# Kernel tuning notes

Measured on AMD Instinct MI355X. Metric: run time of the kernel, lower is better.

Reference implementation:

```python
import jax, jax.numpy as jnp
import numpy as np

D = 512            # model size
H = 8              # num_heads
HD = D // H        # head_size = 64
WIN = 7            # num_keys (payload tokens per window)
QNB = 5            # query_nb for 'mean' aggregation
SCALE = D ** -0.5  # NOTE: torch module scales by size**-0.5, not head_size**-0.5
EPS = 1e-5


def setup_inputs() -> dict:
    key = jax.random.key(0)
    ks = jax.random.split(key, 12)
    B, M = 8, 4096
    w = lambda i: jax.random.normal(ks[i], (D, D), jnp.float32) * 0.02
    return {
        "k": jax.random.normal(ks[0], (B, M, D), jnp.float32),
        "v": jax.random.normal(ks[1], (B, M, D), jnp.float32),
        "q": jax.random.normal(ks[2], (B, M, D), jnp.float32),
        "query_len": 3584,
        "Wk": w(3), "bk": jnp.zeros((D,), jnp.float32),
        "Wv": w(4), "bv": jnp.zeros((D,), jnp.float32),
        "Wq": w(5), "bq": jnp.zeros((D,), jnp.float32),
        "ln_g": jnp.ones((D,), jnp.float32), "ln_b": jnp.zeros((D,), jnp.float32),
        "Wpq": w(6), "bpq": jnp.zeros((D,), jnp.float32),
        "Wpk": w(7), "bpk": jnp.zeros((D,), jnp.float32),
        "Wo": w(8), "bo": jnp.zeros((D,), jnp.float32),
    }


def reference(k, v, q, query_len, Wk, bk, Wv, bv, Wq, bq, ln_g, ln_b, Wpq, bpq, Wpk, bpk, Wo, bo):
    B, M, _ = k.shape
    win_num = -(-query_len // WIN)     # ceil
    per_win = M // win_num

    k = k @ Wk + bk
    v = v @ Wv + bv
    q = q @ Wq + bq

    # 'mean' query aggregation: AvgPool1d(kernel=QNB, stride=1, pad=QNB//2),
    # count_include_pad=True => always divide by QNB (zero-padded)
    qp = jnp.pad(q, ((0, 0), (QNB // 2, QNB // 2), (0, 0)))
    q = sum(qp[:, j:j + M] for j in range(QNB)) / QNB

    # ---- stage 1: DSA (local attention inside each window of per_win tokens)
    resh = lambda x: x.reshape(B, win_num, per_win, H, HD).transpose(0, 1, 3, 2, 4)
    dq, dk, dv = resh(q), resh(k), resh(v)                       # [B,W,H,p,hd]
    attn = jax.nn.softmax(jnp.einsum('bwhqd,bwhkd->bwhqk', dq, dk) * SCALE, axis=-1)
    out = jnp.einsum('bwhqk,bwhkd->bwhqd', attn, dv)
    out = out.transpose(0, 1, 3, 2, 4).reshape(B, win_num, per_win, D)

    win_tok = out[:, :, 0, :]          # [B, W, D] window summary tokens
    attn_x = out[:, :, 1:, :]

    # LayerNorm + exact GELU on window tokens
    mu = win_tok.mean(-1, keepdims=True)
    var = ((win_tok - mu) ** 2).mean(-1, keepdims=True)
    win_tok = (win_tok - mu) / jnp.sqrt(var + EPS) * ln_g + ln_b
    win_tok = jax.nn.gelu(win_tok, approximate=False)

    # ---- stage 2: PSA (attention over window summary tokens)
    pq = (win_tok @ Wpq + bpq).reshape(B, win_num, H, HD).transpose(0, 2, 1, 3)  # [B,H,W,hd]
    pk = (win_tok @ Wpk + bpk).reshape(B, win_num, H, HD).transpose(0, 2, 1, 3)
    pv = attn_x.reshape(B, win_num, WIN, H, HD).transpose(0, 3, 1, 2, 4)
    pv = pv.reshape(B, H, win_num, WIN * HD)

    pattn = jax.nn.softmax(jnp.einsum('bhqd,bhkd->bhqk', pq, pk) * SCALE, axis=-1)
    pout = jnp.einsum('bhqk,bhkd->bhqd', pattn, pv)
    pout = pout.transpose(0, 2, 1, 3).reshape(B, win_num, H, WIN, HD)
    pout = pout.transpose(0, 1, 3, 2, 4).reshape(B, win_num, WIN, D)

    out = (pout + attn_x).reshape(B, win_num * WIN, D)[:, :query_len, :]
    return out @ Wo + bo
```

## Files before the change

kernel.cpp:

```cpp
#include <hip/hip_runtime.h>
#include <hip/hip_bf16.h>
#include <math.h>

#define SCALE_ 0.04419417382415922f
#define EPS_  1e-5f

typedef unsigned short u16;
typedef __attribute__((ext_vector_type(8))) short     bf16x8;
typedef __attribute__((ext_vector_type(4))) float     f32x4;
typedef __attribute__((ext_vector_type(8))) unsigned short u16x8;
typedef __attribute__((ext_vector_type(4))) unsigned short u16x4;

__device__ __forceinline__ u16 f2b(float f) {
  union { float f; unsigned int u; } x; x.f = f;
  unsigned int u = x.u;
  return (u16)((u + 0x7FFFu + ((u >> 16) & 1u)) >> 16);
}
__device__ __forceinline__ float b2f(u16 h) {
  union { unsigned int u; float f; } x; x.u = ((unsigned int)h) << 16;
  return x.f;
}
__device__ __forceinline__ void gload_lds16(const void* g, void* l) {
  __builtin_amdgcn_global_load_lds(
      (const __attribute__((address_space(1))) void*)g,
      (__attribute__((address_space(3))) void*)l, 16, 0, 0);
}

__global__ __launch_bounds__(256) void wconv(
    const float* W0, const float* W1, const float* W2,
    const float* W3, const float* W4, const float* W5, u16* wt)
{
  const float* W;
  switch (blockIdx.z) {
    case 0: W = W0; break; case 1: W = W1; break; case 2: W = W2; break;
    case 3: W = W3; break; case 4: W = W4; break; default: W = W5; break;
  }
  u16* Wt = wt + (size_t)blockIdx.z * 262144;
  const int k0 = blockIdx.x * 64, n0 = blockIdx.y * 64;
  __shared__ float T[64][68];
  const int tid = threadIdx.x;
#pragma unroll
  for (int it = 0; it < 4; ++it) {
    int L = it * 256 + tid;
    int r = L >> 4, cg = L & 15;
    float4 v = *reinterpret_cast<const float4*>(W + (size_t)(k0 + r) * 512 + n0 + cg * 4);
    T[r][cg * 4 + 0] = v.x; T[r][cg * 4 + 1] = v.y;
    T[r][cg * 4 + 2] = v.z; T[r][cg * 4 + 3] = v.w;
  }
  __syncthreads();
#pragma unroll
  for (int it = 0; it < 2; ++it) {
    int L = it * 256 + tid;
    int rn = L >> 3, kg = L & 7;
    u16x8 o;
#pragma unroll
    for (int e = 0; e < 8; ++e) o[e] = f2b(T[kg * 8 + e][rn]);
    *(u16x8*)(Wt + (size_t)(n0 + rn) * 512 + k0 + kg * 8) = o;
  }
}

__global__ __launch_bounds__(512) void gemm_proj(
    const float* A0, const u16* Bt0, const float* bi0, u16* C0,
    const float* A1, const u16* Bt1, const float* bi1, u16* C1,
    const float* A2, const u16* Bt2, const float* bi2, u16* C2)
{
  const float *A, *bias; const u16* Bt; u16* C;
  if (blockIdx.z == 0)      { A = A0; Bt = Bt0; bias = bi0; C = C0; }
  else if (blockIdx.z == 1) { A = A1; Bt = Bt1; bias = bi1; C = C1; }
  else                      { A = A2; Bt = Bt2; bias = bi2; C = C2; }

  __shared__ u16 As[8192];
  __shared__ u16 Bs[32768];
  const int tid = threadIdx.x;
  const int lane = tid & 63, wid = tid >> 6;
  const int wr = wid >> 2, wcn = wid & 3;
  const int l15 = lane & 15, lh = lane >> 4, l7 = lane & 7;
  const int m0 = blockIdx.x * 128;

  const f32x4 fz = {0.f, 0.f, 0.f, 0.f};
  f32x4 acc[4][8];
#pragma unroll
  for (int m = 0; m < 4; ++m)
#pragma unroll
    for (int n = 0; n < 8; ++n) acc[m][n] = fz;

  int aoff[2], boff[2];
#pragma unroll
  for (int kh = 0; kh < 2; ++kh) {
    int slot = ((kh * 4 + lh) ^ l7) << 4;
    aoff[kh] = (wr * 64 + l15) * 128 + slot;
    boff[kh] = (wcn * 128 + l15) * 128 + slot;
  }

  for (int k0 = 0; k0 < 512; k0 += 64) {
    __syncthreads();
#pragma unroll
    for (int it = 0; it < 8; ++it) {
      int L = it * 512 + tid;
      int r = L >> 3, s = L & 7;
      int c = s ^ (r & 7);
      gload_lds16(Bt + (size_t)r * 512 + k0 + c * 8,
                  (char*)Bs + (it * 512 + wid * 64) * 16);
    }
    float4 xa[2], xb[2];
#pragma unroll
    for (int it = 0; it < 2; ++it) {
      int L = it * 512 + tid;
      int r = L >> 3, s = L & 7;
      int c = s ^ (r & 7);
      const float* ga = A + (size_t)(m0 + r) * 512 + k0 + c * 8;
      xa[it] = *reinterpret_cast<const float4*>(ga);
      xb[it] = *reinterpret_cast<const float4*>(ga + 4);
    }
#pragma unroll
    for (int it = 0; it < 2; ++it) {
      int L = it * 512 + tid;
      u16x8 o;
      o[0] = f2b(xa[it].x); o[1] = f2b(xa[it].y);
      o[2] = f2b(xa[it].z); o[3] = f2b(xa[it].w);
      o[4] = f2b(xb[it].x); o[5] = f2b(xb[it].y);
      o[6] = f2b(xb[it].z); o[7] = f2b(xb[it].w);
      *(u16x8*)((char*)As + L * 16) = o;
    }
    __syncthreads();
#pragma unroll
    for (int kh = 0; kh < 2; ++kh) {
      bf16x8 af[4], bfr[8];
#pragma unroll
      for (int m = 0; m < 4; ++m)
        af[m] = *(const bf16x8*)((const char*)As + aoff[kh] + m * 2048);
#pragma unroll
      for (int n = 0; n < 8; ++n)
        bfr[n] = *(const bf16x8*)((const char*)Bs + boff[kh] + n * 2048);
#pragma unroll
      for (int m = 0; m < 4; ++m)
#pragma unroll
        for (int n = 0; n < 8; ++n)
          acc[m][n] = __builtin_amdgcn_mfma_f32_16x16x32_bf16(af[m], bfr[n], acc[m][n], 0, 0, 0);
    }
  }

  const int gn0 = wcn * 128 + l15;
  float bv[8];
#pragma unroll
  for (int n = 0; n < 8; ++n) bv[n] = bias[gn0 + n * 16];
#pragma unroll
  for (int m = 0; m < 4; ++m)
#pragma unroll
    for (int reg = 0; reg < 4; ++reg) {
      int gm = m0 + wr * 64 + m * 16 + lh * 4 + reg;
#pragma unroll
      for (int n = 0; n < 8; ++n)
        C[(size_t)gm * 512 + gn0 + n * 16] = f2b(acc[m][n][reg] + bv[n]);
    }
}

__global__ __launch_bounds__(512) void gemm_out(
    const u16* __restrict__ A, const u16* __restrict__ Bt,
    const float* __restrict__ bias, float* __restrict__ C)
{
  __shared__ u16 As[2][4096];
  __shared__ u16 Bs[2][16384];
  const int tid = threadIdx.x;
  const int lane = tid & 63, wid = tid >> 6;
  const int wr = wid >> 2, wcn = wid & 3;
  const int l15 = lane & 15, lh = lane >> 4;
  const int sx = (l15 >> 1) & 3;
  const int m0 = blockIdx.x * 128;
  const int rr = tid >> 2, sp = tid & 3;
  const int ssw = sp ^ ((rr >> 1) & 3);

  const f32x4 fz = {0.f, 0.f, 0.f, 0.f};
  f32x4 acc[4][8];
#pragma unroll
  for (int m = 0; m < 4; ++m)
#pragma unroll
    for (int n = 0; n < 8; ++n) acc[m][n] = fz;

  const int aoff0 = (wr * 64 + l15) * 64 + ((lh ^ sx) << 4);
  const int boff0 = (wcn * 128 + l15) * 64 + ((lh ^ sx) << 4);

  {
#pragma unroll
    for (int it = 0; it < 4; ++it)
      gload_lds16(Bt + (size_t)(it * 128 + rr) * 512 + ssw * 8,
                  (char*)Bs[0] + (it * 512 + wid * 64) * 16);
    gload_lds16(A + (size_t)(m0 + rr) * 512 + ssw * 8,
                (char*)As[0] + (wid * 64) * 16);
  }
  __syncthreads();

#pragma unroll 2
  for (int t = 0; t < 16; ++t) {
    const int cur = t & 1, nxt = cur ^ 1;
    if (t < 15) {
      const int k0 = (t + 1) * 32;
#pragma unroll
      for (int it = 0; it < 4; ++it)
        gload_lds16(Bt + (size_t)(it * 128 + rr) * 512 + k0 + ssw * 8,
                    (char*)Bs[nxt] + (it * 512 + wid * 64) * 16);
      gload_lds16(A + (size_t)(m0 + rr) * 512 + k0 + ssw * 8,
                  (char*)As[nxt] + (wid * 64) * 16);
    }
    bf16x8 af[4], bfr[8];
#pragma unroll
    for (int m = 0; m < 4; ++m)
      af[m] = *(const bf16x8*)((const char*)As[cur] + aoff0 + m * 1024);
#pragma unroll
    for (int n = 0; n < 8; ++n)
      bfr[n] = *(const bf16x8*)((const char*)Bs[cur] + boff0 + n * 1024);
#pragma unroll
    for (int m = 0; m < 4; ++m)
#pragma unroll
      for (int n = 0; n < 8; ++n)
        acc[m][n] = __builtin_amdgcn_mfma_f32_16x16x32_bf16(af[m], bfr[n], acc[m][n], 0, 0, 0);
    __syncthreads();
  }

  const int gn0 = wcn * 128 + l15;
  float bv[8];
#pragma unroll
  for (int n = 0; n < 8; ++n) bv[n] = bias[gn0 + n * 16];
#pragma unroll
  for (int m = 0; m < 4; ++m)
#pragma unroll
    for (int reg = 0; reg < 4; ++reg) {
      int gm = m0 + wr * 64 + m * 16 + lh * 4 + reg;
#pragma unroll
      for (int n = 0; n < 8; ++n)
        C[(size_t)gm * 512 + gn0 + n * 16] = acc[m][n][reg] + bv[n];
    }
}

__global__ __launch_bounds__(256) void gemm_pp(
    const u16* __restrict__ A,
    const u16* __restrict__ Bt0, const float* __restrict__ bi0, u16* __restrict__ C0,
    const u16* __restrict__ Bt1, const float* __restrict__ bi1, u16* __restrict__ C1)
{
  const u16* Bt; const float* bias; u16* C;
  if (blockIdx.z == 0) { Bt = Bt0; bias = bi0; C = C0; }
  else                 { Bt = Bt1; bias = bi1; C = C1; }

  __shared__ u16 As[8192];
  __shared__ u16 Bs[8192];
  const int tid = threadIdx.x;
  const int lane = tid & 63, wid = tid >> 6;
  const int wr = wid >> 1, wc = wid & 1;
  const int l15 = lane & 15, lh = lane >> 4, l7 = lane & 7;
  const int m0 = blockIdx.x * 128, n0 = blockIdx.y * 128;

  const f32x4 fz = {0.f, 0.f, 0.f, 0.f};
  f32x4 acc[4][4];
#pragma unroll
  for (int m = 0; m < 4; ++m)
#pragma unroll
    for (int n = 0; n < 4; ++n) acc[m][n] = fz;

  int aoff[2], boff[2];
#pragma unroll
  for (int kh = 0; kh < 2; ++kh) {
    int slot = ((kh * 4 + lh) ^ l7) << 4;
    aoff[kh] = (wr * 64 + l15) * 128 + slot;
    boff[kh] = (wc * 64 + l15) * 128 + slot;
  }

  for (int k0 = 0; k0 < 512; k0 += 64) {
    __syncthreads();
#pragma unroll
    for (int it = 0; it < 4; ++it) {
      int L = it * 256 + tid;
      int r = L >> 3, s = L & 7;
      int c = s ^ (r & 7);
      gload_lds16(A  + (size_t)(m0 + r) * 512 + k0 + c * 8,
                  (char*)As + (it * 256 + wid * 64) * 16);
      gload_lds16(Bt + (size_t)(n0 + r) * 512 + k0 + c * 8,
                  (char*)Bs + (it * 256 + wid * 64) * 16);
    }
    __syncthreads();
#pragma unroll
    for (int kh = 0; kh < 2; ++kh) {
      bf16x8 af[4], bfr[4];
#pragma unroll
      for (int m = 0; m < 4; ++m)
        af[m] = *(const bf16x8*)((const char*)As + aoff[kh] + m * 2048);
#pragma unroll
      for (int n = 0; n < 4; ++n)
        bfr[n] = *(const bf16x8*)((const char*)Bs + boff[kh] + n * 2048);
#pragma unroll
      for (int m = 0; m < 4; ++m)
#pragma unroll
        for (int n = 0; n < 4; ++n)
          acc[m][n] = __builtin_amdgcn_mfma_f32_16x16x32_bf16(af[m], bfr[n], acc[m][n], 0, 0, 0);
    }
  }

  const int gn0 = n0 + wc * 64 + l15;
  float bv[4];
#pragma unroll
  for (int n = 0; n < 4; ++n) bv[n] = bias[gn0 + n * 16];
#pragma unroll
  for (int m = 0; m < 4; ++m)
#pragma unroll
    for (int reg = 0; reg < 4; ++reg) {
      int gm = m0 + wr * 64 + m * 16 + lh * 4 + reg;
#pragma unroll
      for (int n = 0; n < 4; ++n)
        C[(size_t)gm * 512 + gn0 + n * 16] = f2b(acc[m][n][reg] + bv[n]);
    }
}

__global__ __launch_bounds__(256) void qk_mfma(
    const u16* __restrict__ pq, const u16* __restrict__ pk, u16* __restrict__ expS)
{
  __shared__ u16 As[8192];
  __shared__ u16 Bs[8192];
  const int tid = threadIdx.x;
  const int lane = tid & 63, wid = tid >> 6;
  const int wr = wid >> 1, wc = wid & 1;
  const int l15 = lane & 15, lh = lane >> 4, l7 = lane & 7;
  const int bh = blockIdx.x & 63;
  const int sidx = blockIdx.x >> 6;
  const int b = bh >> 3, h = bh & 7;
  const int wq0 = (sidx & 3) * 128, wk0 = (sidx >> 2) * 128;

  const f32x4 fz = {0.f, 0.f, 0.f, 0.f};
  f32x4 acc[4][4];
#pragma unroll
  for (int m = 0; m < 4; ++m)
#pragma unroll
    for (int n = 0; n < 4; ++n) acc[m][n] = fz;

#pragma unroll
  for (int it = 0; it < 4; ++it) {
    int L = it * 256 + tid;
    int r = L >> 3, s = L & 7;
    int c = s ^ (r & 7);
    gload_lds16(pq + ((size_t)b * 512 + wq0 + r) * 512 + h * 64 + c * 8,
                (char*)As + (it * 256 + wid * 64) * 16);
    gload_lds16(pk + ((size_t)b * 512 + wk0 + r) * 512 + h * 64 + c * 8,
                (char*)Bs + (it * 256 + wid * 64) * 16);
  }
  __syncthreads();

#pragma unroll
  for (int kh = 0; kh < 2; ++kh) {
    int slot = ((kh * 4 + lh) ^ l7) << 4;
    int aoff = (wr * 64 + l15) * 128 + slot;
    int boff = (wc * 64 + l15) * 128 + slot;
    bf16x8 af[4], bfr[4];
#pragma unroll
    for (int m = 0; m < 4; ++m)
      af[m] = *(const bf16x8*)((const char*)As + aoff + m * 2048);
#pragma unroll
    for (int n = 0; n < 4; ++n)
      bfr[n] = *(const bf16x8*)((const char*)Bs + boff + n * 2048);
#pragma unroll
    for (int m = 0; m < 4; ++m)
#pragma unroll
      for (int n = 0; n < 4; ++n)
        acc[m][n] = __builtin_amdgcn_mfma_f32_16x16x32_bf16(af[m], bfr[n], acc[m][n], 0, 0, 0);
  }

  const int gn0 = wk0 + wc * 64 + l15;
#pragma unroll
  for (int m = 0; m < 4; ++m)
#pragma unroll
    for (int reg = 0; reg < 4; ++reg) {
      int gm = wq0 + wr * 64 + m * 16 + lh * 4 + reg;
#pragma unroll
      for (int n = 0; n < 4; ++n)
        expS[((size_t)bh * 512 + gm) * 512 + gn0 + n * 16] =
            f2b(expf(acc[m][n][reg] * SCALE_));
    }
}

__global__ __launch_bounds__(256) void attn_win(
    const u16* kp, const u16* vp, const u16* qp0, u16* attn)
{
  const int wid = threadIdx.x >> 6;
  const int t = threadIdx.x & 63;
  const int h = blockIdx.x * 4 + wid, w = blockIdx.y, b = blockIdx.z;
  __shared__ float ks[4][8][68], vs[4][8][68], qr[4][12][68], qs[4][8][68], Ps[4][8][9];
  const size_t base = ((size_t)b * 4096 + (size_t)w * 8) * 512 + h * 64;

  {
    int i = t >> 3, dg = t & 7;
    u16x8 kv = *(const u16x8*)(kp + base + (size_t)i * 512 + dg * 8);
    u16x8 vv = *(const u16x8*)(vp + base + (size_t)i * 512 + dg * 8);
#pragma unroll
    for (int e = 0; e < 8; ++e) {
      ks[wid][i][dg * 8 + e] = b2f(kv[e]);
      vs[wid][i][dg * 8 + e] = b2f(vv[e]);
    }
  }
#pragma unroll
  for (int l = 0; l < 2; ++l) {
    int L = t + l * 64;
    if (L < 96) {
      int i = L >> 3, dg = L & 7;
      int m = w * 8 - 2 + i;
      if (m >= 0 && m < 4096) {
        u16x8 qv = *(const u16x8*)(qp0 + ((size_t)b * 4096 + m) * 512 + h * 64 + dg * 8);
#pragma unroll
        for (int e = 0; e < 8; ++e) qr[wid][i][dg * 8 + e] = b2f(qv[e]);
      } else {
#pragma unroll
        for (int e = 0; e < 8; ++e) qr[wid][i][dg * 8 + e] = 0.0f;
      }
    }
  }
  __builtin_amdgcn_s_waitcnt(0);
#pragma unroll
  for (int j = 0; j < 8; ++j)
    qs[wid][j][t] = 0.2f * (qr[wid][j][t] + qr[wid][j + 1][t] + qr[wid][j + 2][t] +
                            qr[wid][j + 3][t] + qr[wid][j + 4][t]);
  __builtin_amdgcn_s_waitcnt(0);

  const int qi = t >> 3, kj = t & 7;
  float s = 0.0f;
#pragma unroll
  for (int d = 0; d < 64; ++d) s = fmaf(qs[wid][qi][d], ks[wid][kj][d], s);
  s *= SCALE_;
  float mx = s;
  mx = fmaxf(mx, __shfl_xor(mx, 1));
  mx = fmaxf(mx, __shfl_xor(mx, 2));
  mx = fmaxf(mx, __shfl_xor(mx, 4));
  float e = expf(s - mx);
  float sum = e;
  sum += __shfl_xor(sum, 1);
  sum += __shfl_xor(sum, 2);
  sum += __shfl_xor(sum, 4);
  Ps[wid][qi][kj] = e / sum;
  __builtin_amdgcn_s_waitcnt(0);

  float o[8];
#pragma unroll
  for (int c = 0; c < 8; ++c) o[c] = 0.0f;
#pragma unroll
  for (int tt = 0; tt < 8; ++tt) {
    float pw = Ps[wid][qi][tt];
#pragma unroll
    for (int c = 0; c < 8; ++c) o[c] = fmaf(pw, vs[wid][tt][kj * 8 + c], o[c]);
  }
  u16x8 ov;
#pragma unroll
  for (int c = 0; c < 8; ++c) ov[c] = f2b(o[c]);
  *(u16x8*)(attn + base + (size_t)qi * 512 + kj * 8) = ov;
}

__global__ __launch_bounds__(256) void pvt_build(const u16* attn, u16* pvT)
{
  const int bh = blockIdx.x;
  const int b = bh >> 3, h = bh & 7;
  const int w0 = blockIdx.y * 32;
  __shared__ u16 TL[448 * 40];
  const int tid = threadIdx.x;
#pragma unroll
  for (int it = 0; it < 8; ++it) {
    int L = it * 256 + tid;
    int dg = L & 7, r = L >> 3;
    int w2l = r >> 3, tt = r & 7;
    if (tt < 7) {
      int m = 8 * (w0 + w2l) + tt + 1;
      u16x8 v = *(const u16x8*)(attn + ((size_t)b * 4096 + m) * 512 + h * 64 + dg * 8);
#pragma unroll
      for (int e = 0; e < 8; ++e)
        TL[(tt * 64 + dg * 8 + e) * 40 + w2l] = v[e];
    }
  }
  __syncthreads();
#pragma unroll
  for (int it = 0; it < 7; ++it) {
    int L = it * 256 + tid;
    int n = L >> 2, seg = L & 3;
    u16x8 v = *(const u16x8*)(&TL[n * 40 + seg * 8]);
    *(u16x8*)(pvT + ((size_t)bh * 448 + n) * 512 + w0 + seg * 8) = v;
  }
}

__global__ __launch_bounds__(64) void ln_gelu(
    const u16* attn, const float* g, const float* be, u16* wt)
{
  const int r = blockIdx.x;
  const int b = r >> 9, w = r & 511;
  const int t = threadIdx.x;
  const u16* x = attn + (((size_t)b * 4096) + (size_t)w * 8) * 512;

  u16x8 v = *(const u16x8*)(x + t * 8);
  float xv[8];
  float s1 = 0.f, s2 = 0.f;
#pragma unroll
  for (int e = 0; e < 8; ++e) {
    xv[e] = b2f(v[e]);
    s1 += xv[e]; s2 += xv[e] * xv[e];
  }
#pragma unroll
  for (int off = 1; off < 64; off <<= 1) {
    s1 += __shfl_xor(s1, off);
    s2 += __shfl_xor(s2, off);
  }
  const float mu  = s1 * (1.0f / 512.0f);
  const float var = s2 * (1.0f / 512.0f) - mu * mu;
  const float inv = 1.0f / sqrtf(var + EPS_);

  const int d0 = t * 8;
  float4 g0 = *reinterpret_cast<const float4*>(g + d0);
  float4 g1 = *reinterpret_cast<const float4*>(g + d0 + 4);
  float4 b0 = *reinterpret_cast<const float4*>(be + d0);
  float4 b1 = *reinterpret_cast<const float4*>(be + d0 + 4);
  float gv[8] = {g0.x, g0.y, g0.z, g0.w, g1.x, g1.y, g1.z, g1.w};
  float bvv[8] = {b0.x, b0.y, b0.z, b0.w, b1.x, b1.y, b1.z, b1.w};
  const float k2 = 0.70710678118654752f;
  u16x8 ov;
#pragma unroll
  for (int e = 0; e < 8; ++e) {
    float y = (xv[e] - mu) * inv * gv[e] + bvv[e];
    ov[e] = f2b(0.5f * y * (1.0f + erff(y * k2)));
  }
  *(u16x8*)(wt + (size_t)r * 512 + d0) = ov;
}

__global__ __launch_bounds__(256) void rs_inv(const u16* expS, float* rsinv)
{
  const int row = blockIdx.x * 4 + (threadIdx.x >> 6);
  const int t = threadIdx.x & 63;
  u16x8 v = *(const u16x8*)(expS + (size_t)row * 512 + t * 8);
  float s = 0.f;
#pragma unroll
  for (int e = 0; e < 8; ++e) s += b2f(v[e]);
#pragma unroll
  for (int off = 1; off < 64; off <<= 1) s += __shfl_xor(s, off);
  if (t == 0) rsinv[row] = 1.0f / s;
}

__global__ __launch_bounds__(256) void pv_mfma(
    const u16* __restrict__ expS, const u16* __restrict__ pvT,
    const float* __restrict__ rsinv, const u16* __restrict__ attn,
    u16* __restrict__ X2)
{
  __shared__ u16 As[8192];
  __shared__ u16 Bs[4096];
  const int tid = threadIdx.x;
  const int lane = tid & 63, wid = tid >> 6;
  const int wr = wid >> 1, wc = wid & 1;
  const int l15 = lane & 15, lh = lane >> 4, l7 = lane & 7;
  const int nt  = blockIdx.x >> 8;
  const int idx = blockIdx.x & 255;
  const int m0 = (idx & 3) * 128;
  const int bh = idx >> 2, b = bh >> 3, h = bh & 7;

  const f32x4 fz = {0.f, 0.f, 0.f, 0.f};
  f32x4 acc[4][2];
#pragma unroll
  for (int m = 0; m < 4; ++m)
#pragma unroll
    for (int n = 0; n < 2; ++n) acc[m][n] = fz;

  int aoff[2], boff[2];
#pragma unroll
  for (int kh = 0; kh < 2; ++kh) {
    int slot = ((kh * 4 + lh) ^ l7) << 4;
    aoff[kh] = (wr * 64 + l15) * 128 + slot;
    boff[kh] = (wc * 32 + l15) * 128 + slot;
  }

  for (int k0 = 0; k0 < 512; k0 += 64) {
    __syncthreads();
#pragma unroll
    for (int it = 0; it < 4; ++it) {
      int L = it * 256 + tid;
      int r = L >> 3, s = L & 7;
      int c = s ^ (r & 7);
      gload_lds16(expS + ((size_t)bh * 512 + m0 + r) * 512 + k0 + c * 8,
                  (char*)As + (it * 256 + wid * 64) * 16);
    }
#pragma unroll
    for (int it = 0; it < 2; ++it) {
      int L = it * 256 + tid;
      int r = L >> 3, s = L & 7;
      int c = s ^ (r & 7);
      gload_lds16(pvT + ((size_t)bh * 448 + nt * 64 + r) * 512 + k0 + c * 8,
                  (char*)Bs + (it * 256 + wid * 64) * 16);
    }
    __syncthreads();
#pragma unroll
    for (int kh = 0; kh < 2; ++kh) {
      bf16x8 af[4], bfr[2];
#pragma unroll
      for (int m = 0; m < 4; ++m)
        af[m] = *(const bf16x8*)((const char*)As + aoff[kh] + m * 2048);
#pragma unroll
      for (int n = 0; n < 2; ++n)
        bfr[n] = *(const bf16x8*)((const char*)Bs + boff[kh] + n * 2048);
#pragma unroll
      for (int m = 0; m < 4; ++m)
#pragma unroll
        for (int n = 0; n < 2; ++n)
          acc[m][n] = __builtin_amdgcn_mfma_f32_16x16x32_bf16(af[m], bfr[n], acc[m][n], 0, 0, 0);
    }
  }

#pragma unroll
  for (int m = 0; m < 4; ++m)
#pragma unroll
    for (int reg = 0; reg < 4; ++reg) {
      int gm = m0 + wr * 64 + m * 16 + lh * 4 + reg;
      float ri = rsinv[bh * 512 + gm];
#pragma unroll
      for (int n = 0; n < 2; ++n) {
        int d = wc * 32 + n * 16 + l15;
        float res = b2f(attn[((size_t)b * 4096 + gm * 8 + nt + 1) * 512 + h * 64 + d]);
        X2[((size_t)b * 3584 + gm * 7 + nt) * 512 + h * 64 + d] =
            f2b(acc[m][n][reg] * ri + res);
      }
    }
}

extern "C" void kernel_launch(void* const* d_in, const int* in_sizes, int n_in,
                              void* d_out, int out_size, void* d_ws, size_t ws_size,
                              hipStream_t stream)
{
  const float* k_in = (const float*)d_in[0];
  const float* v_in = (const float*)d_in[1];
  const float* q_in = (const float*)d_in[2];
  const float* Wk  = (const float*)d_in[4];
  const float* bk  = (const float*)d_in[5];
  const float* Wv  = (const float*)d_in[6];
  const float* bv  = (const float*)d_in[7];
  const float* Wq  = (const float*)d_in[8];
  const float* bq  = (const float*)d_in[9];
  const float* lng = (const float*)d_in[10];
  const float* lnb = (const float*)d_in[11];
  const float* Wpq = (const float*)d_in[12];
  const float* bpq = (const float*)d_in[13];
  const float* Wpk = (const float*)d_in[14];
  const float* bpk = (const float*)d_in[15];
  const float* Wo  = (const float*)d_in[16];
  const float* bo  = (const float*)d_in[17];
  float* out = (float*)d_out;

  char* ws = (char*)d_ws;
  const size_t MB = 1024 * 1024;
  u16* wtb  = (u16*)(ws);
  u16* kp   = (u16*)(ws + 16 * MB);
  u16* vp   = (u16*)(ws + 52 * MB);
  u16* qp0  = (u16*)(ws + 88 * MB);
  u16* attn = (u16*)(ws + 124 * MB);
  u16*   wt    = (u16*)(ws + 16 * MB);
  u16*   pq    = (u16*)(ws + 20 * MB);
  u16*   pk    = (u16*)(ws + 28 * MB);
  float* rsinv = (float*)(ws + 36 * MB);
  u16*   expS  = (u16*)(ws + 40 * MB);
  u16*   pvT   = (u16*)(ws + 76 * MB);
  u16*   X2    = (u16*)(ws + 160 * MB);

  u16* Wkt  = wtb;
  u16* Wvt  = wtb + 1 * 262144;
  u16* Wqt  = wtb + 2 * 262144;
  u16* Wpqt = wtb + 3 * 262144;
  u16* Wpkt = wtb + 4 * 262144;
  u16* Wot  = wtb + 5 * 262144;

  wconv<<<dim3(8, 8, 6), 256, 0, stream>>>(Wk, Wv, Wq, Wpq, Wpk, Wo, wtb);

  gemm_proj<<<dim3(256, 1, 3), 512, 0, stream>>>(
      k_in, Wkt, bk, kp,
      v_in, Wvt, bv, vp,
      q_in, Wqt, bq, qp0);

  attn_win<<<dim3(2, 512, 8), 256, 0, stream>>>(kp, vp, qp0, attn);
  pvt_build<<<dim3(64, 16), 256, 0, stream>>>(attn, pvT);
  ln_gelu<<<4096, 64, 0, stream>>>(attn, lng, lnb, wt);

  gemm_pp<<<dim3(32, 4, 2), 256, 0, stream>>>(
      wt, Wpqt, bpq, pq, Wpkt, bpk, pk);

  qk_mfma<<<1024, 256, 0, stream>>>(pq, pk, expS);
  rs_inv<<<8192, 256, 0, stream>>>(expS, rsinv);
  pv_mfma<<<1792, 256, 0, stream>>>(expS, pvT, rsinv, attn, X2);

  gemm_out<<<dim3(224, 1, 1), 512, 0, stream>>>(X2, Wot, bo, out);
}
```

Measured before the change: 288.1 us.

## Fuse softmax row-sum partials into qk_mfma epilogue; one-wave blocks for attn_win

qk_mfma now keeps row partial sums of the exponentials in fp32 while writing expS, reduces them across the 16-lane groups with shuffles, and stores per-64-column partials. rs_inv then only adds 8 partials per row instead of rereading the whole 32 MB bf16 expS matrix. Separately, attn_win is relaunched as one 64-thread block per head with __syncthreads in place of waitcnt-only ordering. The row sums now come from unrounded fp32 values rather than the bf16-rounded ones, and the shuffles add a little epilogue work.

```diff
diff --git a/kernel.cpp b/kernel.cpp
--- a/kernel.cpp
+++ b/kernel.cpp
@@ -310,7 +310,8 @@
 }
 
 __global__ __launch_bounds__(256) void qk_mfma(
-    const u16* __restrict__ pq, const u16* __restrict__ pk, u16* __restrict__ expS)
+    const u16* __restrict__ pq, const u16* __restrict__ pk,
+    u16* __restrict__ expS, float* __restrict__ rsumP)
 {
   __shared__ u16 As[8192];
   __shared__ u16 Bs[8192];
@@ -362,25 +363,51 @@
   }
 
   const int gn0 = wk0 + wc * 64 + l15;
+  float rs[4][4];
 #pragma unroll
   for (int m = 0; m < 4; ++m)
 #pragma unroll
     for (int reg = 0; reg < 4; ++reg) {
       int gm = wq0 + wr * 64 + m * 16 + lh * 4 + reg;
-#pragma unroll
-      for (int n = 0; n < 4; ++n)
-        expS[((size_t)bh * 512 + gm) * 512 + gn0 + n * 16] =
-            f2b(expf(acc[m][n][reg] * SCALE_));
-    }
-}
-
-__global__ __launch_bounds__(256) void attn_win(
+      float rsum = 0.0f;
+#pragma unroll
+      for (int n = 0; n < 4; ++n) {
+        float e = expf(acc[m][n][reg] * SCALE_);
+        rsum += e;
+        expS[((size_t)bh * 512 + gm) * 512 + gn0 + n * 16] = f2b(e);
+      }
+      rs[m][reg] = rsum;
+    }
+
+#pragma unroll
+  for (int m = 0; m < 4; ++m)
+#pragma unroll
+    for (int reg = 0; reg < 4; ++reg) {
+      float v = rs[m][reg];
+      v += __shfl_xor(v, 1);
+      v += __shfl_xor(v, 2);
+      v += __shfl_xor(v, 4);
+      v += __shfl_xor(v, 8);
+      rs[m][reg] = v;
+    }
+  if (l15 == 0) {
+    const int p = (wk0 >> 6) + wc;
+#pragma unroll
+    for (int m = 0; m < 4; ++m)
+#pragma unroll
+      for (int reg = 0; reg < 4; ++reg) {
+        int gm = wq0 + wr * 64 + m * 16 + lh * 4 + reg;
+        rsumP[((size_t)bh * 8 + p) * 512 + gm] = rs[m][reg];
+      }
+  }
+}
+
+__global__ __launch_bounds__(64) void attn_win(
     const u16* kp, const u16* vp, const u16* qp0, u16* attn)
 {
-  const int wid = threadIdx.x >> 6;
-  const int t = threadIdx.x & 63;
-  const int h = blockIdx.x * 4 + wid, w = blockIdx.y, b = blockIdx.z;
-  __shared__ float ks[4][8][68], vs[4][8][68], qr[4][12][68], qs[4][8][68], Ps[4][8][9];
+  const int h = blockIdx.x, w = blockIdx.y, b = blockIdx.z;
+  const int t = threadIdx.x;
+  __shared__ float ks[8][68], vs[8][68], qr[12][68], qs[8][68], Ps[8][9];
   const size_t base = ((size_t)b * 4096 + (size_t)w * 8) * 512 + h * 64;
 
   {
@@ -389,8 +416,8 @@
     u16x8 vv = *(const u16x8*)(vp + base + (size_t)i * 512 + dg * 8);
 #pragma unroll
     for (int e = 0; e < 8; ++e) {
-      ks[wid][i][dg * 8 + e] = b2f(kv[e]);
-      vs[wid][i][dg * 8 + e] = b2f(vv[e]);
+      ks[i][dg * 8 + e] = b2f(kv[e]);
+      vs[i][dg * 8 + e] = b2f(vv[e]);
     }
   }
 #pragma unroll
@@ -402,24 +429,23 @@
       if (m >= 0 && m < 4096) {
         u16x8 qv = *(const u16x8*)(qp0 + ((size_t)b * 4096 + m) * 512 + h * 64 + dg * 8);
 #pragma unroll
-        for (int e = 0; e < 8; ++e) qr[wid][i][dg * 8 + e] = b2f(qv[e]);
+        for (int e = 0; e < 8; ++e) qr[i][dg * 8 + e] = b2f(qv[e]);
       } else {
 #pragma unroll
-        for (int e = 0; e < 8; ++e) qr[wid][i][dg * 8 + e] = 0.0f;
+        for (int e = 0; e < 8; ++e) qr[i][dg * 8 + e] = 0.0f;
       }
     }
   }
-  __builtin_amdgcn_s_waitcnt(0);
+  __syncthreads();
 #pragma unroll
   for (int j = 0; j < 8; ++j)
-    qs[wid][j][t] = 0.2f * (qr[wid][j][t] + qr[wid][j + 1][t] + qr[wid][j + 2][t] +
-                            qr[wid][j + 3][t] + qr[wid][j + 4][t]);
-  __builtin_amdgcn_s_waitcnt(0);
+    qs[j][t] = 0.2f * (qr[j][t] + qr[j + 1][t] + qr[j + 2][t] + qr[j + 3][t] + qr[j + 4][t]);
+  __syncthreads();
 
   const int qi = t >> 3, kj = t & 7;
   float s = 0.0f;
 #pragma unroll
-  for (int d = 0; d < 64; ++d) s = fmaf(qs[wid][qi][d], ks[wid][kj][d], s);
+  for (int d = 0; d < 64; ++d) s = fmaf(qs[qi][d], ks[kj][d], s);
   s *= SCALE_;
   float mx = s;
   mx = fmaxf(mx, __shfl_xor(mx, 1));
@@ -430,17 +456,17 @@
   sum += __shfl_xor(sum, 1);
   sum += __shfl_xor(sum, 2);
   sum += __shfl_xor(sum, 4);
-  Ps[wid][qi][kj] = e / sum;
-  __builtin_amdgcn_s_waitcnt(0);
+  Ps[qi][kj] = e / sum;
+  __syncthreads();
 
   float o[8];
 #pragma unroll
   for (int c = 0; c < 8; ++c) o[c] = 0.0f;
 #pragma unroll
   for (int tt = 0; tt < 8; ++tt) {
-    float pw = Ps[wid][qi][tt];
-#pragma unroll
-    for (int c = 0; c < 8; ++c) o[c] = fmaf(pw, vs[wid][tt][kj * 8 + c], o[c]);
+    float pw = Ps[qi][tt];
+#pragma unroll
+    for (int c = 0; c < 8; ++c) o[c] = fmaf(pw, vs[tt][kj * 8 + c], o[c]);
   }
   u16x8 ov;
 #pragma unroll
@@ -520,17 +546,15 @@
   *(u16x8*)(wt + (size_t)r * 512 + d0) = ov;
 }
 
-__global__ __launch_bounds__(256) void rs_inv(const u16* expS, float* rsinv)
-{
-  const int row = blockIdx.x * 4 + (threadIdx.x >> 6);
-  const int t = threadIdx.x & 63;
-  u16x8 v = *(const u16x8*)(expS + (size_t)row * 512 + t * 8);
+__global__ __launch_bounds__(256) void rs_inv(const float* rsumP, float* rsinv)
+{
+  const int row = blockIdx.x * 256 + threadIdx.x;
+  const int bh = row >> 9, wq = row & 511;
   float s = 0.f;
 #pragma unroll
-  for (int e = 0; e < 8; ++e) s += b2f(v[e]);
-#pragma unroll
-  for (int off = 1; off < 64; off <<= 1) s += __shfl_xor(s, off);
-  if (t == 0) rsinv[row] = 1.0f / s;
+  for (int p = 0; p < 8; ++p)
+    s += rsumP[((size_t)bh * 8 + p) * 512 + wq];
+  rsinv[row] = 1.0f / s;
 }
 
 __global__ __launch_bounds__(256) void pv_mfma(
@@ -650,6 +674,7 @@
   u16*   pq    = (u16*)(ws + 20 * MB);
   u16*   pk    = (u16*)(ws + 28 * MB);
   float* rsinv = (float*)(ws + 36 * MB);
+  float* rsumP = (float*)(ws + 37 * MB);
   u16*   expS  = (u16*)(ws + 40 * MB);
   u16*   pvT   = (u16*)(ws + 76 * MB);
   u16*   X2    = (u16*)(ws + 160 * MB);
@@ -668,15 +693,15 @@
       v_in, Wvt, bv, vp,
       q_in, Wqt, bq, qp0);
 
-  attn_win<<<dim3(2, 512, 8), 256, 0, stream>>>(kp, vp, qp0, attn);
+  attn_win<<<dim3(8, 512, 8), 64, 0, stream>>>(kp, vp, qp0, attn);
   pvt_build<<<dim3(64, 16), 256, 0, stream>>>(attn, pvT);
   ln_gelu<<<4096, 64, 0, stream>>>(attn, lng, lnb, wt);
 
   gemm_pp<<<dim3(32, 4, 2), 256, 0, stream>>>(
       wt, Wpqt, bpq, pq, Wpkt, bpk, pk);
 
-  qk_mfma<<<1024, 256, 0, stream>>>(pq, pk, expS);
-  rs_inv<<<8192, 256, 0, stream>>>(expS, rsinv);
+  qk_mfma<<<1024, 256, 0, stream>>>(pq, pk, expS, rsumP);
+  rs_inv<<<128, 256, 0, stream>>>(rsumP, rsinv);
   pv_mfma<<<1792, 256, 0, stream>>>(expS, pvT, rsinv, attn, X2);
 
   gemm_out<<<dim3(224, 1, 1), 512, 0, stream>>>(X2, Wot, bo, out);
```

Measured after the change: 278.0 us. -3.5%, faster.
